# Optimization experiments

Hardware: AMD Instinct MI355X
Metric: run time of the kernel (lower is better)

Reference implementation:

```python
import jax, jax.numpy as jnp
import numpy as np

B, S, H, W = 16, 512, 768, 8


def _enumerate_spans(S, W):
    # same enumeration order as the torch triple loop: for i, for j in [i, min(i+W, S)-1]
    starts, widths = [], []
    for i in range(S):
        for w in range(1, min(W, S - i) + 1):
            starts.append(i)
            widths.append(w)
    return np.asarray(starts, np.int32), np.asarray(widths, np.int32)


def setup_inputs() -> dict:
    key = jax.random.key(0)
    k1, k2, k3 = jax.random.split(key, 3)
    embeddings = jax.random.normal(k1, (B, S, H), dtype=jnp.float32)
    w_lin = jax.random.normal(k2, (2 * H + 1, H), dtype=jnp.float32) * 0.02
    b_lin = jax.random.normal(k3, (H,), dtype=jnp.float32) * 0.02
    starts, widths = _enumerate_spans(S, W)
    return {
        "embeddings": embeddings,
        "w_lin": w_lin,
        "b_lin": b_lin,
        "span_starts": jnp.asarray(starts),
        "span_widths": jnp.asarray(widths),
    }


def reference(embeddings, w_lin, b_lin, span_starts, span_widths):
    Bb, Ss, Hh = embeddings.shape
    cls_emb = embeddings[:, 0, :]  # [B, H]

    # Sliding-window running max: pooled[k, b, i, :] = max(embeddings[b, i:i+k+1, :])
    neg = jnp.full((Bb, W - 1, Hh), -jnp.inf, embeddings.dtype)
    padded = jnp.concatenate([embeddings, neg], axis=1)  # [B, S+W-1, H]
    cm = embeddings
    pools = [cm]
    for k in range(1, W):
        cm = jnp.maximum(cm, padded[:, k:k + Ss, :])
        pools.append(cm)
    pooled = jnp.stack(pools, axis=0)  # [W, B, S, H]

    # Gather each span's max-pooled embedding: [N, B, H] -> [B, N, H]
    span_max = pooled[span_widths - 1, :, span_starts, :]
    span_max = jnp.transpose(span_max, (1, 0, 2))

    N = span_starts.shape[0]
    cls_b = jnp.broadcast_to(cls_emb[:, None, :], (Bb, N, Hh))
    width_f = jnp.broadcast_to(
        span_widths.astype(embeddings.dtype)[None, :, None], (Bb, N, 1))
    feats = jnp.concatenate([span_max, cls_b, width_f], axis=-1)  # [B, N, 2H+1]

    span_reps = jnp.einsum("bnf,fh->bnh", feats, w_lin) + b_lin
    token_inputs = cls_emb  # [B, H]
    return token_inputs, span_reps.reshape(Bb * N, Hh)
```

## Files before the change

### kernel.cpp

```cpp
#include <hip/hip_runtime.h>
#include <hip/hip_bf16.h>
#include <stdint.h>

#define AS1 __attribute__((address_space(1)))
#define AS3 __attribute__((address_space(3)))

typedef float  f32x4  __attribute__((ext_vector_type(4)));
typedef __bf16 bf16x8 __attribute__((ext_vector_type(8)));
typedef __bf16 bf16x2 __attribute__((ext_vector_type(2)));
typedef short  s16x8  __attribute__((ext_vector_type(8)));

static constexpr int Bc = 16, Sc = 512, Hc = 768, NSPAN = 4068;
static constexpr int BM = 128, BN = 128, BK = 64, KS = Hc / BK;

static __device__ __forceinline__ uint32_t pack2bf(float x, float y) {
  bf16x2 p;
  p[0] = (__bf16)x;
  p[1] = (__bf16)y;
  return __builtin_bit_cast(uint32_t, p);
}

__global__ __launch_bounds__(256)
void prep_w1t(const float* __restrict__ w_lin, unsigned short* __restrict__ w1t) {
  __shared__ __align__(16) unsigned short T[64][80];
  int bidk = blockIdx.x % 12, bidn = blockIdx.x / 12;
  int k0 = bidk * 64, n0 = bidn * 64;
  int tid = threadIdx.x;
#pragma unroll
  for (int p = 0; p < 16; ++p) {
    int idx = p * 256 + tid;
    int kl = idx >> 6, nl = idx & 63;
    float v = w_lin[(size_t)(k0 + kl) * Hc + (n0 + nl)];
    __bf16 bv = (__bf16)v;
    T[nl][kl] = __builtin_bit_cast(unsigned short, bv);
  }
  __syncthreads();
#pragma unroll
  for (int qq = 0; qq < 2; ++qq) {
    int q = qq * 256 + tid;
    int nl = q >> 3, c = q & 7;
    int n = n0 + nl;
    int gp = (k0 >> 3) + (c ^ (n & 7));
    s16x8 v = *(const s16x8*)(&T[nl][c * 8]);
    *(s16x8*)(w1t + (size_t)n * Hc + gp * 8) = v;
  }
}

__global__ __launch_bounds__(256)
void cls_proj_kernel(const float* __restrict__ emb, const float* __restrict__ w_lin,
                     const float* __restrict__ b_lin, float* __restrict__ out,
                     float* __restrict__ cls_proj) {
  __shared__ float cls_s[Hc];
  int b = blockIdx.x / 3, hc = blockIdx.x % 3;
  int tid = threadIdx.x;
  const float* cls = emb + (size_t)b * Sc * Hc;
  for (int i = tid; i < Hc; i += 256) cls_s[i] = cls[i];
  __syncthreads();
  int h = hc * 256 + tid;
  const float* wp = w_lin + (size_t)Hc * Hc + h;
  float p0 = 0, p1 = 0, p2 = 0, p3 = 0, p4 = 0, p5 = 0, p6 = 0, p7 = 0;
  for (int f = 0; f < Hc; f += 8) {
    p0 += cls_s[f + 0] * wp[(size_t)(f + 0) * Hc];
    p1 += cls_s[f + 1] * wp[(size_t)(f + 1) * Hc];
    p2 += cls_s[f + 2] * wp[(size_t)(f + 2) * Hc];
    p3 += cls_s[f + 3] * wp[(size_t)(f + 3) * Hc];
    p4 += cls_s[f + 4] * wp[(size_t)(f + 4) * Hc];
    p5 += cls_s[f + 5] * wp[(size_t)(f + 5) * Hc];
    p6 += cls_s[f + 6] * wp[(size_t)(f + 6) * Hc];
    p7 += cls_s[f + 7] * wp[(size_t)(f + 7) * Hc];
  }
  float acc = b_lin[h] + (((p0 + p1) + (p2 + p3)) + ((p4 + p5) + (p6 + p7)));
  cls_proj[b * Hc + h] = acc;
  out[b * Hc + h] = cls_s[h];
}

__global__ __launch_bounds__(256, 2)
void span_gemm(const float* __restrict__ emb, const unsigned short* __restrict__ w1t,
               const float* __restrict__ cls_proj, const float* __restrict__ w_lin,
               float* __restrict__ out) {
  __shared__ __align__(16) float embS[24 * 64];
  __shared__ __align__(16) unsigned short Ald[BM * BK];
  __shared__ __align__(16) unsigned short Bld[BN * BK];

  int bid = blockIdx.x;
  int tile_n = bid % 6, tile_m = bid / 6;
  int b = tile_m >> 5;
  int s0 = (tile_m & 31) << 4;
  int n0 = tile_n * BN;
  int tid = threadIdx.x;
  int wid = tid >> 6, lane = tid & 63;
  int wave_m = wid >> 1, wave_n = wid & 1;
  int lq = lane >> 4, lr = lane & 15;

  const float* embB = emb + (size_t)b * Sc * Hc;

  f32x4 acc[4][4];
  f32x4 zer = {0.f, 0.f, 0.f, 0.f};
#pragma unroll
  for (int i = 0; i < 4; ++i)
#pragma unroll
    for (int j = 0; j < 4; ++j) acc[i][j] = zer;

  for (int ks = 0; ks < KS; ++ks) {
    int k0 = ks * BK;
    __syncthreads();

    {
      int t = wid;
      int r = s0 + (t << 2) + lq;
      if (r > 511) r = 511;
      const float* gp = embB + (size_t)r * Hc + k0 + (lr << 2);
      __builtin_amdgcn_global_load_lds((const AS1 uint32_t*)gp,
                                       (AS3 uint32_t*)(embS + (t << 8)), 16, 0, 0);
      if (wid < 2) {
        int t2 = 4 + wid;
        int r2 = s0 + (t2 << 2) + lq;
        if (r2 > 511) r2 = 511;
        const float* gp2 = embB + (size_t)r2 * Hc + k0 + (lr << 2);
        __builtin_amdgcn_global_load_lds((const AS1 uint32_t*)gp2,
                                         (AS3 uint32_t*)(embS + (t2 << 8)), 16, 0, 0);
      }
    }
#pragma unroll
    for (int j = 0; j < 4; ++j) {
      int u = (wid << 2) + j;
      int n = n0 + (u << 3) + (lane >> 3);
      const unsigned short* gp = w1t + (size_t)n * Hc + k0 + ((lane & 7) << 3);
      __builtin_amdgcn_global_load_lds((const AS1 uint32_t*)gp,
                                       (AS3 uint32_t*)(Bld + (u << 9)), 16, 0, 0);
    }
    __syncthreads();

#pragma unroll
    for (int qq = 0; qq < 2; ++qq) {
      int q = (qq << 8) + tid;
      int i = q >> 5, kp = q & 31;
      const float* ebase = embS + (kp << 1);
      float2 cm = *(const float2*)(ebase + (i << 6));
      {
        int mm = i << 3;
        uint32_t pk = pack2bf(cm.x, cm.y);
        int off = (mm << 7) + (((kp >> 2) ^ (mm & 7)) << 4) + ((kp & 3) << 2);
        *(uint32_t*)((char*)Ald + off) = pk;
      }
#pragma unroll
      for (int t = 1; t < 8; ++t) {
        float2 e = *(const float2*)(ebase + ((i + t) << 6));
        cm.x = fmaxf(cm.x, e.x);
        cm.y = fmaxf(cm.y, e.y);
        int mm = (i << 3) + t;
        uint32_t pk = pack2bf(cm.x, cm.y);
        int off = (mm << 7) + (((kp >> 2) ^ (mm & 7)) << 4) + ((kp & 3) << 2);
        *(uint32_t*)((char*)Ald + off) = pk;
      }
    }
    __syncthreads();

#pragma unroll
    for (int kk = 0; kk < 2; ++kk) {
      bf16x8 af[4], bfr[4];
      int cf = (kk << 2) + lq;
#pragma unroll
      for (int mi = 0; mi < 4; ++mi) {
        int m = (wave_m << 6) + (mi << 4) + lr;
        af[mi] = *(const bf16x8*)((const char*)Ald + (m << 7) + ((cf ^ (m & 7)) << 4));
      }
#pragma unroll
      for (int ni = 0; ni < 4; ++ni) {
        int n = (wave_n << 6) + (ni << 4) + lr;
        bfr[ni] = *(const bf16x8*)((const char*)Bld + (n << 7) + ((cf ^ (n & 7)) << 4));
      }
#pragma unroll
      for (int mi = 0; mi < 4; ++mi)
#pragma unroll
        for (int ni = 0; ni < 4; ++ni)
          acc[mi][ni] = __builtin_amdgcn_mfma_f32_16x16x32_bf16(af[mi], bfr[ni], acc[mi][ni], 0, 0, 0);
    }
  }

  const float* w2p = w_lin + (size_t)(2 * Hc) * Hc;
  float* outp = out + Bc * Hc;
  int mb0 = tile_m << 7;
#pragma unroll
  for (int ni = 0; ni < 4; ++ni) {
    int h = n0 + (wave_n << 6) + (ni << 4) + lr;
    float cp = cls_proj[b * Hc + h];
    float w2 = w2p[h];
#pragma unroll
    for (int mi = 0; mi < 4; ++mi) {
#pragma unroll
      for (int j = 0; j < 4; ++j) {
        int mg = mb0 + (wave_m << 6) + (mi << 4) + (lq << 2) + j;
        int sw = mg & 4095;
        int s = sw >> 3, w = (sw & 7) + 1;
        if (s + w <= 512) {
          int nsp = (s <= 504) ? ((s << 3) + w - 1)
                               : (NSPAN - (((512 - s) * (513 - s)) >> 1) + w - 1);
          size_t oidx = ((size_t)b * NSPAN + nsp) * Hc + h;
          outp[oidx] = acc[mi][ni][j] + cp + (float)w * w2;
        }
      }
    }
  }
}

extern "C" void kernel_launch(void* const* d_in, const int* in_sizes, int n_in,
                              void* d_out, int out_size, void* d_ws, size_t ws_size,
                              hipStream_t stream) {
  const float* emb = (const float*)d_in[0];
  const float* w_lin = (const float*)d_in[1];
  const float* b_lin = (const float*)d_in[2];
  unsigned short* w1t = (unsigned short*)d_ws;
  float* cls_proj = (float*)((char*)d_ws + (size_t)Hc * Hc * 2);
  float* out = (float*)d_out;

  hipLaunchKernelGGL(prep_w1t, dim3(144), dim3(256), 0, stream, w_lin, w1t);
  hipLaunchKernelGGL(cls_proj_kernel, dim3(48), dim3(256), 0, stream, emb, w_lin, b_lin, out, cls_proj);
  hipLaunchKernelGGL(span_gemm, dim3(512 * 6), dim3(256), 0, stream, emb, w1t, cls_proj, w_lin, out);
}
```

Baseline: 139.3 us.

## Widen span GEMM N tile and compute running max directly from registers

The span GEMM tile grows from 128x128 to 128x256, and each wave now covers all 128 rows and 64 columns, so half as many blocks recompute the sliding-window max and the A operand is reused more. Embedding rows are loaded straight into registers with vector global loads, and the running max plus bf16 packing happen in registers. This removes the LDS staging buffer for embeddings and one barrier per k-step. The cost is a doubled accumulator array (32 f32x4 per thread), which raises register pressure and may lower occupancy under the launch bound of 2 blocks. The global loads are also no longer asynchronous into LDS.

```diff
diff --git a/kernel.cpp b/kernel.cpp
--- a/kernel.cpp
+++ b/kernel.cpp
@@ -7,18 +7,11 @@
 
 typedef float  f32x4  __attribute__((ext_vector_type(4)));
 typedef __bf16 bf16x8 __attribute__((ext_vector_type(8)));
-typedef __bf16 bf16x2 __attribute__((ext_vector_type(2)));
+typedef __bf16 bf16x4 __attribute__((ext_vector_type(4)));
 typedef short  s16x8  __attribute__((ext_vector_type(8)));
 
 static constexpr int Bc = 16, Sc = 512, Hc = 768, NSPAN = 4068;
-static constexpr int BM = 128, BN = 128, BK = 64, KS = Hc / BK;
-
-static __device__ __forceinline__ uint32_t pack2bf(float x, float y) {
-  bf16x2 p;
-  p[0] = (__bf16)x;
-  p[1] = (__bf16)y;
-  return __builtin_bit_cast(uint32_t, p);
-}
+static constexpr int BM = 128, BN = 256, BK = 64, KS = Hc / BK;
 
 __global__ __launch_bounds__(256)
 void prep_w1t(const float* __restrict__ w_lin, unsigned short* __restrict__ w1t) {
@@ -78,100 +71,92 @@
 void span_gemm(const float* __restrict__ emb, const unsigned short* __restrict__ w1t,
                const float* __restrict__ cls_proj, const float* __restrict__ w_lin,
                float* __restrict__ out) {
-  __shared__ __align__(16) float embS[24 * 64];
   __shared__ __align__(16) unsigned short Ald[BM * BK];
   __shared__ __align__(16) unsigned short Bld[BN * BK];
 
   int bid = blockIdx.x;
-  int tile_n = bid % 6, tile_m = bid / 6;
+  int tile_n = bid % 3, tile_m = bid / 3;
   int b = tile_m >> 5;
   int s0 = (tile_m & 31) << 4;
   int n0 = tile_n * BN;
   int tid = threadIdx.x;
   int wid = tid >> 6, lane = tid & 63;
-  int wave_m = wid >> 1, wave_n = wid & 1;
   int lq = lane >> 4, lr = lane & 15;
 
-  const float* embB = emb + (size_t)b * Sc * Hc;
-
-  f32x4 acc[4][4];
+  const char* embC = (const char*)(emb + (size_t)b * Sc * Hc);
+
+  int bi = tid >> 4, bkq = tid & 15;
+  uint32_t rowoff[8];
+#pragma unroll
+  for (int t = 0; t < 8; ++t) {
+    int r = s0 + bi + t;
+    if (r > 511) r = 511;
+    rowoff[t] = (uint32_t)r * (Hc * 4) + bkq * 16;
+  }
+  int awbase = (bi << 10) + ((bkq & 1) << 3);
+
+  f32x4 acc[8][4];
   f32x4 zer = {0.f, 0.f, 0.f, 0.f};
 #pragma unroll
-  for (int i = 0; i < 4; ++i)
+  for (int i = 0; i < 8; ++i)
 #pragma unroll
     for (int j = 0; j < 4; ++j) acc[i][j] = zer;
 
   for (int ks = 0; ks < KS; ++ks) {
     int k0 = ks * BK;
+
+    f32x4 rv[8];
+#pragma unroll
+    for (int t = 0; t < 8; ++t)
+      rv[t] = *(const f32x4*)(embC + rowoff[t] + k0 * 4);
+
     __syncthreads();
 
-    {
-      int t = wid;
-      int r = s0 + (t << 2) + lq;
-      if (r > 511) r = 511;
-      const float* gp = embB + (size_t)r * Hc + k0 + (lr << 2);
-      __builtin_amdgcn_global_load_lds((const AS1 uint32_t*)gp,
-                                       (AS3 uint32_t*)(embS + (t << 8)), 16, 0, 0);
-      if (wid < 2) {
-        int t2 = 4 + wid;
-        int r2 = s0 + (t2 << 2) + lq;
-        if (r2 > 511) r2 = 511;
-        const float* gp2 = embB + (size_t)r2 * Hc + k0 + (lr << 2);
-        __builtin_amdgcn_global_load_lds((const AS1 uint32_t*)gp2,
-                                         (AS3 uint32_t*)(embS + (t2 << 8)), 16, 0, 0);
-      }
-    }
-#pragma unroll
-    for (int j = 0; j < 4; ++j) {
-      int u = (wid << 2) + j;
+#pragma unroll
+    for (int j = 0; j < 8; ++j) {
+      int u = (wid << 3) + j;
       int n = n0 + (u << 3) + (lane >> 3);
       const unsigned short* gp = w1t + (size_t)n * Hc + k0 + ((lane & 7) << 3);
       __builtin_amdgcn_global_load_lds((const AS1 uint32_t*)gp,
                                        (AS3 uint32_t*)(Bld + (u << 9)), 16, 0, 0);
     }
+
+    {
+      f32x4 cm = rv[0];
+#pragma unroll
+      for (int t = 0; t < 8; ++t) {
+        if (t) {
+          cm[0] = fmaxf(cm[0], rv[t][0]);
+          cm[1] = fmaxf(cm[1], rv[t][1]);
+          cm[2] = fmaxf(cm[2], rv[t][2]);
+          cm[3] = fmaxf(cm[3], rv[t][3]);
+        }
+        bf16x4 p;
+        p[0] = (__bf16)cm[0]; p[1] = (__bf16)cm[1];
+        p[2] = (__bf16)cm[2]; p[3] = (__bf16)cm[3];
+        int off = awbase + (t << 7) + ((((bkq >> 1) ^ t)) << 4);
+        *(uint2*)((char*)Ald + off) = __builtin_bit_cast(uint2, p);
+      }
+    }
+
     __syncthreads();
 
 #pragma unroll
-    for (int qq = 0; qq < 2; ++qq) {
-      int q = (qq << 8) + tid;
-      int i = q >> 5, kp = q & 31;
-      const float* ebase = embS + (kp << 1);
-      float2 cm = *(const float2*)(ebase + (i << 6));
-      {
-        int mm = i << 3;
-        uint32_t pk = pack2bf(cm.x, cm.y);
-        int off = (mm << 7) + (((kp >> 2) ^ (mm & 7)) << 4) + ((kp & 3) << 2);
-        *(uint32_t*)((char*)Ald + off) = pk;
-      }
-#pragma unroll
-      for (int t = 1; t < 8; ++t) {
-        float2 e = *(const float2*)(ebase + ((i + t) << 6));
-        cm.x = fmaxf(cm.x, e.x);
-        cm.y = fmaxf(cm.y, e.y);
-        int mm = (i << 3) + t;
-        uint32_t pk = pack2bf(cm.x, cm.y);
-        int off = (mm << 7) + (((kp >> 2) ^ (mm & 7)) << 4) + ((kp & 3) << 2);
-        *(uint32_t*)((char*)Ald + off) = pk;
-      }
-    }
-    __syncthreads();
-
-#pragma unroll
     for (int kk = 0; kk < 2; ++kk) {
-      bf16x8 af[4], bfr[4];
+      bf16x8 af[8], bfr[4];
       int cf = (kk << 2) + lq;
 #pragma unroll
-      for (int mi = 0; mi < 4; ++mi) {
-        int m = (wave_m << 6) + (mi << 4) + lr;
+      for (int mi = 0; mi < 8; ++mi) {
+        int m = (mi << 4) + lr;
         af[mi] = *(const bf16x8*)((const char*)Ald + (m << 7) + ((cf ^ (m & 7)) << 4));
       }
 #pragma unroll
       for (int ni = 0; ni < 4; ++ni) {
-        int n = (wave_n << 6) + (ni << 4) + lr;
+        int n = (wid << 6) + (ni << 4) + lr;
         bfr[ni] = *(const bf16x8*)((const char*)Bld + (n << 7) + ((cf ^ (n & 7)) << 4));
       }
 #pragma unroll
-      for (int mi = 0; mi < 4; ++mi)
+      for (int mi = 0; mi < 8; ++mi)
 #pragma unroll
         for (int ni = 0; ni < 4; ++ni)
           acc[mi][ni] = __builtin_amdgcn_mfma_f32_16x16x32_bf16(af[mi], bfr[ni], acc[mi][ni], 0, 0, 0);
@@ -180,21 +165,21 @@
 
   const float* w2p = w_lin + (size_t)(2 * Hc) * Hc;
   float* outp = out + Bc * Hc;
-  int mb0 = tile_m << 7;
+  int swb = (tile_m & 31) << 7;
 #pragma unroll
   for (int ni = 0; ni < 4; ++ni) {
-    int h = n0 + (wave_n << 6) + (ni << 4) + lr;
+    int h = n0 + (wid << 6) + (ni << 4) + lr;
     float cp = cls_proj[b * Hc + h];
     float w2 = w2p[h];
 #pragma unroll
-    for (int mi = 0; mi < 4; ++mi) {
+    for (int mi = 0; mi < 8; ++mi) {
 #pragma unroll
       for (int j = 0; j < 4; ++j) {
-        int mg = mb0 + (wave_m << 6) + (mi << 4) + (lq << 2) + j;
-        int sw = mg & 4095;
+        int m = (mi << 4) + (lq << 2) + j;
+        int sw = swb + m;
         int s = sw >> 3, w = (sw & 7) + 1;
         if (s + w <= 512) {
-          int nsp = (s <= 504) ? ((s << 3) + w - 1)
+          int nsp = (s <= 504) ? (sw)
                                : (NSPAN - (((512 - s) * (513 - s)) >> 1) + w - 1);
           size_t oidx = ((size_t)b * NSPAN + nsp) * Hc + h;
           outp[oidx] = acc[mi][ni][j] + cp + (float)w * w2;
@@ -216,5 +201,5 @@
 
   hipLaunchKernelGGL(prep_w1t, dim3(144), dim3(256), 0, stream, w_lin, w1t);
   hipLaunchKernelGGL(cls_proj_kernel, dim3(48), dim3(256), 0, stream, emb, w_lin, b_lin, out, cls_proj);
-  hipLaunchKernelGGL(span_gemm, dim3(512 * 6), dim3(256), 0, stream, emb, w1t, cls_proj, w_lin, out);
-}
+  hipLaunchKernelGGL(span_gemm, dim3(512 * 3), dim3(256), 0, stream, emb, w1t, cls_proj, w_lin, out);
+}
```

Measured after the change: 127.5 us. -8.5%, faster.
